# Kernel optimization log

Hardware: AMD Instinct MI355X
Metric: run time of the kernel (lower is better)

The kernel has to match this reference:

```python
import jax, jax.numpy as jnp
import numpy as np

NUM_USER, BATCH, NUM_NT = 8, 16384, 128
T = 0.3  # SE threshold from the original module


def setup_inputs() -> dict:
    key = jax.random.key(0)
    k1, k2 = jax.random.split(key)
    h = jax.random.normal(k1, (NUM_USER, BATCH, NUM_NT), dtype=jnp.float32)
    v = jax.random.normal(k2, (NUM_USER, BATCH, NUM_NT), dtype=jnp.float32)
    N = jnp.ones((), dtype=jnp.float32)
    return {"h": h, "v": v, "N": N}


def reference(h, v, N):
    num_user, batch, num_nt = h.shape
    d = num_nt // 2
    # split real/imag halves into complex views
    h_c = jax.lax.complex(h[..., :d], h[..., d:])  # (user, batch, d)
    v_c = jax.lax.complex(v[..., :d], v[..., d:])  # (user, batch, d)
    # per-sample Frobenius norm over (user, d) and power scaling to sqrt(num_user)
    norms = jnp.sqrt(jnp.sum(jnp.real(v_c) ** 2 + jnp.imag(v_c) ** 2, axis=(0, 2)))  # (batch,)
    scale = jnp.sqrt(jnp.float32(num_user)) / norms
    v_scaled = v_c * scale[None, :, None]
    # signal: diag(h_user @ v_user^H) per sample == row-wise complex dot, with SCALED v
    S = jnp.abs(jnp.sum(h_c * jnp.conj(v_scaled), axis=-1)) ** 2  # (user, batch)
    # interference: original uses UNSCALED v[j] (faithful to source)
    A = jnp.einsum('ibt,jbt->ijb', h_c, jnp.conj(v_c))  # (user_i, user_j, batch)
    Iall = jnp.abs(A) ** 2
    Ip = jnp.sum(Iall, axis=1) - jnp.einsum('iib->ib', Iall)  # exclude j == i
    SINR = S / (Ip + N)
    R_user = jnp.log2(1.0 + SINR)  # (user, batch)
    R_per_user_p = jnp.mean(R_user, axis=1)  # (user,)
    # Rp = sum_i ( -R_user_i + 10^(T - R_user_i) ) per sample
    Rp = jnp.sum(10.0 ** (T - R_user) - R_user, axis=0)  # (batch,)
    return jnp.mean(Rp), R_per_user_p, jnp.sum(R_per_user_p)
```

## Files before the change

### kernel.cpp

```cpp
#include <hip/hip_runtime.h>
#include <hip/hip_bf16.h>


constexpr int U_    = 8;
constexpr int B_    = 16384;
constexpr int NT_   = 128;
constexpr int D_    = 64;
constexpr int ROWP_ = 132;
constexpr int NBLK_ = 1024;
constexpr int WPB_  = 4;
constexpr int TW_   = NBLK_ * WPB_;
constexpr int IT_   = B_ / TW_;
constexpr float T_THRESH = 0.3f;
constexpr float LOG2_10  = 3.3219280948873623f;

__device__ __forceinline__ float waveReduceSum(float v) {
    #pragma unroll
    for (int m = 1; m < 64; m <<= 1) v += __shfl_xor(v, m, 64);
    return v;
}

__device__ __forceinline__ float hw_log2(float x) { return __builtin_amdgcn_logf(x); }
__device__ __forceinline__ float hw_exp2(float x) { return __builtin_amdgcn_exp2f(x); }

__global__ __launch_bounds__(256, 4) void se_main(const float* __restrict__ h,
                                                  const float* __restrict__ vv,
                                                  const float* __restrict__ Np,
                                                  float* __restrict__ partial) {
    __shared__ float lds[WPB_][2][U_ * ROWP_];
    __shared__ float red_f[WPB_];
    __shared__ float red_R[WPB_][U_];

    const int tid  = threadIdx.x;
    const int wave = tid >> 6;
    const int lane = tid & 63;
    const int ui   = lane >> 3;
    const int uj   = lane & 7;
    const float Nval = Np[0];

    float* hb = lds[wave][0];
    float* vb = lds[wave][1];

    float lane_sumR = 0.0f;
    float lane_sumf = 0.0f;

    const int gwave = blockIdx.x * WPB_ + wave;

    for (int it = 0; it < IT_; ++it) {
        const int b = gwave + it * TW_;

        float nsq = 0.0f;
        #pragma unroll
        for (int t = 0; t < 4; ++t) {
            const int idx = t * 64 + lane;
            const int row = idx >> 5;
            const int c4  = idx & 31;
            const size_t goff = (size_t)row * ((size_t)B_ * NT_) + (size_t)b * NT_ + (size_t)c4 * 4;
            const float4 h4 = *reinterpret_cast<const float4*>(h  + goff);
            const float4 v4 = *reinterpret_cast<const float4*>(vv + goff);
            *reinterpret_cast<float4*>(&hb[row * ROWP_ + c4 * 4]) = h4;
            *reinterpret_cast<float4*>(&vb[row * ROWP_ + c4 * 4]) = v4;
            nsq += v4.x * v4.x + v4.y * v4.y + v4.z * v4.z + v4.w * v4.w;
        }
        const float normsq = waveReduceSum(nsq);

        float are = 0.0f, aim = 0.0f;
        const float* hrow = &hb[ui * ROWP_];
        const float* vrow = &vb[uj * ROWP_];
        #pragma unroll
        for (int k = 0; k < D_; k += 4) {
            const float4 hr = *reinterpret_cast<const float4*>(hrow + k);
            const float4 hi = *reinterpret_cast<const float4*>(hrow + D_ + k);
            const float4 vr = *reinterpret_cast<const float4*>(vrow + k);
            const float4 vi = *reinterpret_cast<const float4*>(vrow + D_ + k);
            are += hr.x * vr.x + hi.x * vi.x;
            aim += hi.x * vr.x - hr.x * vi.x;
            are += hr.y * vr.y + hi.y * vi.y;
            aim += hi.y * vr.y - hr.y * vi.y;
            are += hr.z * vr.z + hi.z * vi.z;
            aim += hi.z * vr.z - hr.z * vi.z;
            are += hr.w * vr.w + hi.w * vi.w;
            aim += hi.w * vr.w - hr.w * vi.w;
        }
        const float Iall = are * are + aim * aim;

        const float diag = __shfl(Iall, ui * 9, 64);
        float rowsum = Iall;
        rowsum += __shfl_xor(rowsum, 1, 64);
        rowsum += __shfl_xor(rowsum, 2, 64);
        rowsum += __shfl_xor(rowsum, 4, 64);

        const float Ip   = rowsum - diag;
        const float S    = (8.0f / normsq) * diag;
        const float SINR = S / (Ip + Nval);
        const float R    = hw_log2(1.0f + SINR);

        lane_sumR += R;
        lane_sumf += hw_exp2((T_THRESH - R) * LOG2_10) - R;
    }

    const float wf = waveReduceSum(lane_sumf) * 0.125f;
    if (lane == 0) red_f[wave] = wf;
    if (uj == 0)   red_R[wave][ui] = lane_sumR;
    __syncthreads();

    if (tid < U_) {
        float s = 0.0f;
        #pragma unroll
        for (int w = 0; w < WPB_; ++w) s += red_R[w][tid];
        partial[blockIdx.x * 9 + 1 + tid] = s;
    } else if (tid == U_) {
        float s = 0.0f;
        #pragma unroll
        for (int w = 0; w < WPB_; ++w) s += red_f[w];
        partial[blockIdx.x * 9] = s;
    }
}

__global__ __launch_bounds__(256) void se_final(const float* __restrict__ partial,
                                                float* __restrict__ out) {
    __shared__ float sums[9];
    if (threadIdx.x < 9) sums[threadIdx.x] = 0.0f;
    __syncthreads();

    float local[9];
    #pragma unroll
    for (int s = 0; s < 9; ++s) local[s] = 0.0f;
    for (int b = threadIdx.x; b < NBLK_; b += 256) {
        #pragma unroll
        for (int s = 0; s < 9; ++s) local[s] += partial[b * 9 + s];
    }
    #pragma unroll
    for (int s = 0; s < 9; ++s) atomicAdd(&sums[s], local[s]);
    __syncthreads();

    if (threadIdx.x == 0) {
        const float inv = 1.0f / (float)B_;
        out[0] = sums[0] * inv;
        float tot = 0.0f;
        #pragma unroll
        for (int i = 0; i < U_; ++i) {
            const float r = sums[1 + i] * inv;
            out[1 + i] = r;
            tot += r;
        }
        out[9] = tot;
    }
}

extern "C" void kernel_launch(void* const* d_in, const int* in_sizes, int n_in,
                              void* d_out, int out_size, void* d_ws, size_t ws_size,
                              hipStream_t stream) {
    const float* h  = (const float*)d_in[0];
    const float* v  = (const float*)d_in[1];
    const float* Np = (const float*)d_in[2];
    float* out      = (float*)d_out;
    float* partial  = (float*)d_ws;

    se_main<<<NBLK_, 256, 0, stream>>>(h, v, Np, partial);
    se_final<<<1, 256, 0, stream>>>(partial, out);
}
```

Before: 169.4 us.

## Use packed FMA math, interleave norm reduction, and launch one block per wave-sample

The grid grows from 1024 to up to 4096 blocks, sized by the workspace, so each wave handles a single sample instead of looping over four. The complex dot products and the norm accumulation now use two-wide vector FMAs that can map to packed fp32 instructions. The norm wave-reduction is interleaved with the row-sum shuffles to overlap their latency. The larger grid exposes more parallelism for the loads but gives up the per-wave loop that could overlap memory across iterations, and it makes the final reduction read more partials.

Result: slower. 173.6 us (+2.5%).

```diff
diff --git a/kernel.cpp b/kernel.cpp
--- a/kernel.cpp
+++ b/kernel.cpp
@@ -1,24 +1,18 @@
 #include <hip/hip_runtime.h>
 #include <hip/hip_bf16.h>
 
+
+typedef float v2f __attribute__((ext_vector_type(2)));
 
 constexpr int U_    = 8;
 constexpr int B_    = 16384;
 constexpr int NT_   = 128;
 constexpr int D_    = 64;
 constexpr int ROWP_ = 132;
-constexpr int NBLK_ = 1024;
 constexpr int WPB_  = 4;
-constexpr int TW_   = NBLK_ * WPB_;
-constexpr int IT_   = B_ / TW_;
+constexpr int NBLK_MAX = 4096;
 constexpr float T_THRESH = 0.3f;
 constexpr float LOG2_10  = 3.3219280948873623f;
-
-__device__ __forceinline__ float waveReduceSum(float v) {
-    #pragma unroll
-    for (int m = 1; m < 64; m <<= 1) v += __shfl_xor(v, m, 64);
-    return v;
-}
 
 __device__ __forceinline__ float hw_log2(float x) { return __builtin_amdgcn_logf(x); }
 __device__ __forceinline__ float hw_exp2(float x) { return __builtin_amdgcn_exp2f(x); }
@@ -45,11 +39,10 @@
     float lane_sumf = 0.0f;
 
     const int gwave = blockIdx.x * WPB_ + wave;
+    const int totw  = gridDim.x * WPB_;
 
-    for (int it = 0; it < IT_; ++it) {
-        const int b = gwave + it * TW_;
-
-        float nsq = 0.0f;
+    for (int b = gwave; b < B_; b += totw) {
+        v2f nsq2 = {0.0f, 0.0f};
         #pragma unroll
         for (int t = 0; t < 4; ++t) {
             const int idx = t * 64 + lane;
@@ -60,11 +53,13 @@
             const float4 v4 = *reinterpret_cast<const float4*>(vv + goff);
             *reinterpret_cast<float4*>(&hb[row * ROWP_ + c4 * 4]) = h4;
             *reinterpret_cast<float4*>(&vb[row * ROWP_ + c4 * 4]) = v4;
-            nsq += v4.x * v4.x + v4.y * v4.y + v4.z * v4.z + v4.w * v4.w;
+            const v2f va = {v4.x, v4.y}, vb2 = {v4.z, v4.w};
+            nsq2 = __builtin_elementwise_fma(va,  va,  nsq2);
+            nsq2 = __builtin_elementwise_fma(vb2, vb2, nsq2);
         }
-        const float normsq = waveReduceSum(nsq);
+        float nsq = nsq2[0] + nsq2[1];
 
-        float are = 0.0f, aim = 0.0f;
+        v2f are2 = {0.0f, 0.0f}, aim2 = {0.0f, 0.0f};
         const float* hrow = &hb[ui * ROWP_];
         const float* vrow = &vb[uj * ROWP_];
         #pragma unroll
@@ -73,25 +68,34 @@
             const float4 hi = *reinterpret_cast<const float4*>(hrow + D_ + k);
             const float4 vr = *reinterpret_cast<const float4*>(vrow + k);
             const float4 vi = *reinterpret_cast<const float4*>(vrow + D_ + k);
-            are += hr.x * vr.x + hi.x * vi.x;
-            aim += hi.x * vr.x - hr.x * vi.x;
-            are += hr.y * vr.y + hi.y * vi.y;
-            aim += hi.y * vr.y - hr.y * vi.y;
-            are += hr.z * vr.z + hi.z * vi.z;
-            aim += hi.z * vr.z - hr.z * vi.z;
-            are += hr.w * vr.w + hi.w * vi.w;
-            aim += hi.w * vr.w - hr.w * vi.w;
+            const v2f hra = {hr.x, hr.y}, hrb = {hr.z, hr.w};
+            const v2f hia = {hi.x, hi.y}, hib = {hi.z, hi.w};
+            const v2f vra = {vr.x, vr.y}, vrb = {vr.z, vr.w};
+            const v2f via = {vi.x, vi.y}, vib = {vi.z, vi.w};
+            are2 = __builtin_elementwise_fma(hra,  vra, are2);
+            are2 = __builtin_elementwise_fma(hia,  via, are2);
+            aim2 = __builtin_elementwise_fma(hia,  vra, aim2);
+            aim2 = __builtin_elementwise_fma(-hra, via, aim2);
+            are2 = __builtin_elementwise_fma(hrb,  vrb, are2);
+            are2 = __builtin_elementwise_fma(hib,  vib, are2);
+            aim2 = __builtin_elementwise_fma(hib,  vrb, aim2);
+            aim2 = __builtin_elementwise_fma(-hrb, vib, aim2);
         }
+        const float are  = are2[0] + are2[1];
+        const float aim  = aim2[0] + aim2[1];
         const float Iall = are * are + aim * aim;
 
         const float diag = __shfl(Iall, ui * 9, 64);
         float rowsum = Iall;
-        rowsum += __shfl_xor(rowsum, 1, 64);
-        rowsum += __shfl_xor(rowsum, 2, 64);
-        rowsum += __shfl_xor(rowsum, 4, 64);
+        rowsum += __shfl_xor(rowsum, 1, 64);  nsq += __shfl_xor(nsq, 1, 64);
+        rowsum += __shfl_xor(rowsum, 2, 64);  nsq += __shfl_xor(nsq, 2, 64);
+        rowsum += __shfl_xor(rowsum, 4, 64);  nsq += __shfl_xor(nsq, 4, 64);
+        nsq += __shfl_xor(nsq, 8,  64);
+        nsq += __shfl_xor(nsq, 16, 64);
+        nsq += __shfl_xor(nsq, 32, 64);
 
         const float Ip   = rowsum - diag;
-        const float S    = (8.0f / normsq) * diag;
+        const float S    = (8.0f / nsq) * diag;
         const float SINR = S / (Ip + Nval);
         const float R    = hw_log2(1.0f + SINR);
 
@@ -99,7 +103,10 @@
         lane_sumf += hw_exp2((T_THRESH - R) * LOG2_10) - R;
     }
 
-    const float wf = waveReduceSum(lane_sumf) * 0.125f;
+    float wf = lane_sumf;
+    #pragma unroll
+    for (int m = 1; m < 64; m <<= 1) wf += __shfl_xor(wf, m, 64);
+    wf *= 0.125f;
     if (lane == 0) red_f[wave] = wf;
     if (uj == 0)   red_R[wave][ui] = lane_sumR;
     __syncthreads();
@@ -118,7 +125,7 @@
 }
 
 __global__ __launch_bounds__(256) void se_final(const float* __restrict__ partial,
-                                                float* __restrict__ out) {
+                                                float* __restrict__ out, int nblk) {
     __shared__ float sums[9];
     if (threadIdx.x < 9) sums[threadIdx.x] = 0.0f;
     __syncthreads();
@@ -126,7 +133,7 @@
     float local[9];
     #pragma unroll
     for (int s = 0; s < 9; ++s) local[s] = 0.0f;
-    for (int b = threadIdx.x; b < NBLK_; b += 256) {
+    for (int b = threadIdx.x; b < nblk; b += 256) {
         #pragma unroll
         for (int s = 0; s < 9; ++s) local[s] += partial[b * 9 + s];
     }
@@ -157,6 +164,13 @@
     float* out      = (float*)d_out;
     float* partial  = (float*)d_ws;
 
-    se_main<<<NBLK_, 256, 0, stream>>>(h, v, Np, partial);
-    se_final<<<1, 256, 0, stream>>>(partial, out);
+    int nblk = NBLK_MAX;
+    const size_t need = (size_t)NBLK_MAX * 9 * sizeof(float);
+    if (ws_size < need) {
+        nblk = (int)(ws_size / (9 * sizeof(float)));
+        if (nblk < 1) nblk = 1;
+    }
+
+    se_main<<<nblk, 256, 0, stream>>>(h, v, Np, partial);
+    se_final<<<1, 256, 0, stream>>>(partial, out, nblk);
 }
```
